# Performance work log

Measured on AMD Instinct MI355X. Metric: run time of the kernel, lower is better.

Reference implementation:

```python
import jax, jax.numpy as jnp
import numpy as np

RES = 1024
DEPTH = 2.0

def setup_inputs() -> dict:
    key = jax.random.key(0)
    k1, k2 = jax.random.split(key)
    point_cloud = jax.random.normal(k1, (32, 200000, 3), dtype=jnp.float32)
    transformation_matrices = jax.random.normal(k2, (32, 3, 4), dtype=jnp.float32)
    return {"point_cloud": point_cloud, "transformation_matrices": transformation_matrices}

def reference(point_cloud, transformation_matrices):
    B, N, _ = point_cloud.shape
    R = RES
    # homogeneous transform: (B,N,4) @ (B,4,3) -> (B,N,3)
    ones = jnp.ones((B, N, 1), dtype=point_cloud.dtype)
    pc_h = jnp.concatenate([point_cloud, ones], axis=2)
    transformed = jnp.einsum('bnk,bck->bnc', pc_h, transformation_matrices)  # (B,N,3)
    normalized = transformed / DEPTH
    # pixel coords, clamped to [0, R-1]; torch int() truncates (== floor for >=0)
    px = jnp.clip((normalized[:, :, 0] + 1.0) / 2.0 * R, 0.0, R - 1)
    py = jnp.clip((1.0 - normalized[:, :, 1]) / 2.0 * R, 0.0, R - 1)
    xi = jnp.floor(px).astype(jnp.int32)
    yi = jnp.floor(py).astype(jnp.int32)
    z = normalized[:, :, 2]
    b_ids = jnp.arange(B, dtype=jnp.int32)[:, None]
    flat_pix = (b_ids * (R * R) + yi * R + xi).reshape(-1)           # (B*N,)
    gidx = jnp.arange(B * N, dtype=jnp.int32)                        # global point index; within a batch row, larger gidx == larger j
    winners = jax.ops.segment_max(gidx, flat_pix, num_segments=B * R * R)
    valid = winners >= 0                                             # empty segments get int32 min
    safe_w = jnp.clip(winners, 0)
    depth_flat = jnp.where(valid, z.reshape(-1)[safe_w], 0.0)
    depth_map = depth_flat.reshape(B, R, R)
    # F.interpolate to the same (R,R) size with bilinear/align_corners=False is the identity map.
    return depth_map
```

## Files before the change

### kernel.cpp

```cpp
#include <hip/hip_runtime.h>

#define RES   1024
#define NPTS  200000
#define NB    32
#define PPT   8
#define BLK   512
#define NBLK  49
#define BPB   4096
#define NBAND 256
#define BANDH 4
#define BORD  4096
#define NBUCK (NB*NBAND)
#define TGRID 1024

#define OFF_AR 0
#define OFF_TM 51380224
#define OFF_BW 52985856

__global__ __launch_bounds__(256) void k_init(int4* __restrict__ bwin4)
{
    int i = blockIdx.x * 256 + threadIdx.x;
    bwin4[i] = make_int4(-1, -1, -1, -1);
}

__global__ __launch_bounds__(BLK) void k_bin(
        const float* __restrict__ pc,
        const float* __restrict__ tm,
        unsigned long long* __restrict__ arena,
        unsigned int* __restrict__ tmeta,
        int* __restrict__ bwin)
{
#pragma clang fp contract(off)
    const int b   = blockIdx.y;
    const int tid = threadIdx.x;
    const int gg  = b * NBLK + blockIdx.x;

    __shared__ int sb[BORD];
    __shared__ unsigned long long stage[BPB];
    __shared__ unsigned int hist[NBAND];
    __shared__ unsigned int lofs[NBAND];
    for (int k = tid; k < BORD; k += BLK) sb[k] = -1;
    if (tid < NBAND) hist[tid] = 0u;
    __syncthreads();

    const float* M = tm + b * 12;
    const float m0 = M[0], m1 = M[1], m2  = M[2],  m3  = M[3];
    const float m4 = M[4], m5 = M[5], m6  = M[6],  m7  = M[7];
    const float m8 = M[8], m9 = M[9], m10 = M[10], m11 = M[11];

    unsigned long long ent[PPT];
    unsigned int rb[PPT];
    const int base = blockIdx.x * BPB + tid;

    #pragma unroll
    for (int k = 0; k < PPT; ++k) {
        rb[k] = 0xFFFFFFFFu;
        int n = base + k * BLK;
        if (n < NPTS) {
            const float* p = pc + ((size_t)b * NPTS + n) * 3;
            float x = p[0], y = p[1], z = p[2];
            float tx = (x * m0 + y * m1) + (z * m2  + m3);
            float ty = (x * m4 + y * m5) + (z * m6  + m7);
            float tz = (x * m8 + y * m9) + (z * m10 + m11);
            float nx = tx * 0.5f;
            float ny = ty * 0.5f;
            float nz = tz * 0.5f;
            float px = (nx + 1.0f) * 512.0f;
            float py = (1.0f - ny) * 512.0f;
            px = fminf(fmaxf(px, 0.0f), 1023.0f);
            py = fminf(fmaxf(py, 0.0f), 1023.0f);
            int xi = (int)floorf(px);
            int yi = (int)floorf(py);

            bool border = (xi == 0) | (xi == 1023) | (yi == 0) | (yi == 1023);
            if (border) {
                int idx = (yi == 0)    ? xi
                        : (yi == 1023) ? 1024 + xi
                        : (xi == 0)    ? 2048 + yi
                                       : 3072 + yi;
                atomicMax(&sb[idx], n);
            } else {
                int bin = yi >> 2;
                unsigned r = atomicAdd(&hist[bin], 1u);
                rb[k] = ((unsigned)bin << 12) | r;
                unsigned pix = (unsigned)((yi & 3) * RES + xi);
                ent[k] = ((unsigned long long)pix << 52)
                       | ((unsigned long long)(unsigned)n << 32)
                       | (unsigned long long)__float_as_uint(nz);
            }
        }
    }
    __syncthreads();

    if (tid < 64) {
        unsigned carry = 0;
        #pragma unroll
        for (int c = 0; c < 4; ++c) {
            unsigned v = hist[c * 64 + tid];
            unsigned s = v;
            #pragma unroll
            for (int d = 1; d < 64; d <<= 1) {
                unsigned o = __shfl_up(s, d);
                if (tid >= d) s += o;
            }
            lofs[c * 64 + tid] = (s - v) + carry;
            carry += __shfl(s, 63);
        }
    }
    __syncthreads();

    if (tid < NBAND)
        tmeta[((size_t)(b * NBAND + tid)) * NBLK + blockIdx.x]
            = (lofs[tid] << 16) | hist[tid];

    #pragma unroll
    for (int k = 0; k < PPT; ++k) {
        if (rb[k] != 0xFFFFFFFFu) {
            unsigned bin = rb[k] >> 12, r = rb[k] & 4095u;
            stage[lofs[bin] + r] = ent[k];
        }
    }
    __syncthreads();

    const unsigned Ttot = lofs[NBAND - 1] + hist[NBAND - 1];
    for (unsigned k = tid; k < Ttot; k += BLK)
        arena[(size_t)gg * BPB + k] = stage[k];

    for (int k = tid; k < BORD; k += BLK) {
        int v = sb[k];
        if (v >= 0) atomicMax(&bwin[b * BORD + k], v);
    }
}

__global__ __launch_bounds__(512) void k_tile(
        const unsigned long long* __restrict__ arena,
        const unsigned int* __restrict__ tmeta,
        const int* __restrict__ bwin,
        const float* __restrict__ pc,
        const float* __restrict__ tm,
        float* __restrict__ out)
{
#pragma clang fp contract(off)
    const int tid = threadIdx.x;

    __shared__ __align__(16) unsigned long long tile[BANDH * RES];
    __shared__ unsigned int pref[NBLK + 1];
    __shared__ unsigned int sbase[NBLK];

    for (int bucket = blockIdx.x; bucket < NBUCK; bucket += TGRID) {
        const int b = bucket >> 8, band = bucket & 255;

        for (int k = tid; k < BANDH * RES; k += 512) tile[k] = 0ull;

        unsigned mv = 0;
        if (tid < NBLK)
            mv = tmeta[((size_t)(b * NBAND + band)) * NBLK + tid];
        if (tid < 64) {
            unsigned cnt = (tid < NBLK) ? (mv & 0xFFFFu) : 0u;
            unsigned s = cnt;
            #pragma unroll
            for (int d = 1; d < 64; d <<= 1) {
                unsigned o = __shfl_up(s, d);
                if (tid >= d) s += o;
            }
            if (tid < NBLK) {
                pref[tid + 1] = s;
                sbase[tid] = (unsigned)((b * NBLK + tid) * BPB) + (mv >> 16);
            }
            if (tid == 0) pref[0] = 0u;
        }
        __syncthreads();

        const unsigned T = pref[NBLK];
        for (unsigned idx = tid; idx < T; idx += 512) {
            int lo = 0, hi = NBLK - 1;
            #pragma unroll
            for (int it = 0; it < 6; ++it) {
                int mid = (lo + hi + 1) >> 1;
                if (pref[mid] <= idx) lo = mid; else hi = mid - 1;
            }
            unsigned long long e = arena[(size_t)sbase[lo] + (idx - pref[lo])];
            atomicMax(&tile[e >> 52], e & 0x000FFFFFFFFFFFFFull);
        }
        __syncthreads();

        const float* M2 = tm + b * 12 + 8;
        const float m8 = M2[0], m9 = M2[1], m10 = M2[2], m11 = M2[3];
        const int y0 = band * BANDH;
        const int* bw = bwin + b * BORD;

        for (int r = 0; r < BANDH; ++r) {
            int yi = y0 + r;
            ulonglong2 kk = ((const ulonglong2*)(tile + r * RES))[tid];
            unsigned zx = (unsigned)(kk.x & 0xFFFFFFFFull);
            unsigned zy = (unsigned)(kk.y & 0xFFFFFFFFull);

            #pragma unroll
            for (int h = 0; h < 2; ++h) {
                int xi = tid * 2 + h;
                bool isb = (yi == 0) | (yi == 1023) | (xi == 0) | (xi == 1023);
                if (isb) {
                    int n = (yi == 0)    ? bw[xi]
                          : (yi == 1023) ? bw[1024 + xi]
                          : (xi == 0)    ? bw[2048 + yi]
                                         : bw[3072 + yi];
                    float zv = 0.0f;
                    if (n >= 0) {
                        const float* p = pc + ((size_t)b * NPTS + n) * 3;
                        float t = (p[0] * m8 + p[1] * m9) + (p[2] * m10 + m11);
                        zv = t * 0.5f;
                    }
                    if (h) zy = __float_as_uint(zv); else zx = __float_as_uint(zv);
                }
            }
            unsigned long long pv = ((unsigned long long)zy << 32) | zx;
            __builtin_nontemporal_store(pv,
                (unsigned long long*)(out + ((size_t)b * RES + yi) * RES) + tid);
        }
        __syncthreads();
    }
}

extern "C" void kernel_launch(void* const* d_in, const int* in_sizes, int n_in,
                              void* d_out, int out_size, void* d_ws, size_t ws_size,
                              hipStream_t stream)
{
    const float* pc = (const float*)d_in[0];
    const float* tm = (const float*)d_in[1];
    float* out = (float*)d_out;

    char* ws = (char*)d_ws;
    unsigned long long* arena = (unsigned long long*)(ws + OFF_AR);
    unsigned int* tmeta = (unsigned int*)(ws + OFF_TM);
    int*          bwin  = (int*)         (ws + OFF_BW);

    k_init<<<(NB * BORD / 4) / 256, 256, 0, stream>>>((int4*)bwin);

    dim3 g1(NBLK, NB);
    k_bin<<<g1, BLK, 0, stream>>>(pc, tm, arena, tmeta, bwin);

    k_tile<<<TGRID, 512, 0, stream>>>(arena, tmeta, bwin, pc, tm, out);
}
```

Measured before the change: 96.87 us.

## Stage point cloud through shared memory with float4 loads; one tile block per bucket

k_bin now copies each block's points into shared memory with coalesced float4 loads instead of strided 12-byte per-thread loads. It overlays the border-winner array and the staging buffer on one 48KB buffer, and defers the border atomics until after the histogram pass. k_tile drops its grid-stride loop and launches one block per (batch, band) bucket, which adds blocks but removes the serialized iterations. The tradeoff is an extra shared-memory pass and more block launches in exchange for better global load coalescing.

```diff
diff --git a/kernel.cpp b/kernel.cpp
--- a/kernel.cpp
+++ b/kernel.cpp
@@ -10,12 +10,13 @@
 #define NBAND 256
 #define BANDH 4
 #define BORD  4096
-#define NBUCK (NB*NBAND)
-#define TGRID 1024
 
 #define OFF_AR 0
 #define OFF_TM 51380224
 #define OFF_BW 52985856
+
+#define RB_INVALID 0xFFFFFFFFu
+#define RB_BORDER  0xFFFFFFFEu
 
 __global__ __launch_bounds__(256) void k_init(int4* __restrict__ bwin4)
 {
@@ -35,11 +36,22 @@
     const int tid = threadIdx.x;
     const int gg  = b * NBLK + blockIdx.x;
 
-    __shared__ int sb[BORD];
-    __shared__ unsigned long long stage[BPB];
+    __shared__ __align__(16) char smem[49152];
     __shared__ unsigned int hist[NBAND];
     __shared__ unsigned int lofs[NBAND];
-    for (int k = tid; k < BORD; k += BLK) sb[k] = -1;
+
+    float*              pcs   = (float*)smem;
+    float4*             pcs4  = (float4*)smem;
+    int*                sb    = (int*)smem;
+    unsigned long long* stage = (unsigned long long*)(smem + 16384);
+
+    const int blk0     = blockIdx.x * BPB;
+    const int npts_blk = min(BPB, NPTS - blk0);
+    const float* pcb   = pc + (size_t)b * NPTS * 3;
+
+    const int nf4 = (npts_blk * 3) >> 2;
+    const float4* src4 = (const float4*)pcb + ((size_t)blk0 * 3 >> 2);
+    for (int i = tid; i < nf4; i += BLK) pcs4[i] = src4[i];
     if (tid < NBAND) hist[tid] = 0u;
     __syncthreads();
 
@@ -50,15 +62,13 @@
 
     unsigned long long ent[PPT];
     unsigned int rb[PPT];
-    const int base = blockIdx.x * BPB + tid;
 
     #pragma unroll
     for (int k = 0; k < PPT; ++k) {
-        rb[k] = 0xFFFFFFFFu;
-        int n = base + k * BLK;
-        if (n < NPTS) {
-            const float* p = pc + ((size_t)b * NPTS + n) * 3;
-            float x = p[0], y = p[1], z = p[2];
+        rb[k] = RB_INVALID;
+        int j = k * BLK + tid;
+        if (j < npts_blk) {
+            float x = pcs[j * 3], y = pcs[j * 3 + 1], z = pcs[j * 3 + 2];
             float tx = (x * m0 + y * m1) + (z * m2  + m3);
             float ty = (x * m4 + y * m5) + (z * m6  + m7);
             float tz = (x * m8 + y * m9) + (z * m10 + m11);
@@ -71,6 +81,7 @@
             py = fminf(fmaxf(py, 0.0f), 1023.0f);
             int xi = (int)floorf(px);
             int yi = (int)floorf(py);
+            int n  = blk0 + j;
 
             bool border = (xi == 0) | (xi == 1023) | (yi == 0) | (yi == 1023);
             if (border) {
@@ -78,7 +89,8 @@
                         : (yi == 1023) ? 1024 + xi
                         : (xi == 0)    ? 2048 + yi
                                        : 3072 + yi;
-                atomicMax(&sb[idx], n);
+                rb[k]  = RB_BORDER;
+                ent[k] = ((unsigned long long)(unsigned)idx << 32) | (unsigned)n;
             } else {
                 int bin = yi >> 2;
                 unsigned r = atomicAdd(&hist[bin], 1u);
@@ -92,6 +104,7 @@
     }
     __syncthreads();
 
+    for (int k2 = tid; k2 < BORD; k2 += BLK) sb[k2] = -1;
     if (tid < 64) {
         unsigned carry = 0;
         #pragma unroll
@@ -109,26 +122,27 @@
     }
     __syncthreads();
 
+    #pragma unroll
+    for (int k = 0; k < PPT; ++k) {
+        if (rb[k] == RB_BORDER) {
+            atomicMax(&sb[(int)(ent[k] >> 32)], (int)(unsigned)ent[k]);
+        } else if (rb[k] != RB_INVALID) {
+            unsigned bin = rb[k] >> 12, r = rb[k] & 4095u;
+            stage[lofs[bin] + r] = ent[k];
+        }
+    }
     if (tid < NBAND)
         tmeta[((size_t)(b * NBAND + tid)) * NBLK + blockIdx.x]
             = (lofs[tid] << 16) | hist[tid];
-
-    #pragma unroll
-    for (int k = 0; k < PPT; ++k) {
-        if (rb[k] != 0xFFFFFFFFu) {
-            unsigned bin = rb[k] >> 12, r = rb[k] & 4095u;
-            stage[lofs[bin] + r] = ent[k];
-        }
-    }
     __syncthreads();
 
     const unsigned Ttot = lofs[NBAND - 1] + hist[NBAND - 1];
-    for (unsigned k = tid; k < Ttot; k += BLK)
-        arena[(size_t)gg * BPB + k] = stage[k];
-
-    for (int k = tid; k < BORD; k += BLK) {
-        int v = sb[k];
-        if (v >= 0) atomicMax(&bwin[b * BORD + k], v);
+    for (unsigned k2 = tid; k2 < Ttot; k2 += BLK)
+        arena[(size_t)gg * BPB + k2] = stage[k2];
+
+    for (int k2 = tid; k2 < BORD; k2 += BLK) {
+        int v = sb[k2];
+        if (v >= 0) atomicMax(&bwin[b * BORD + k2], v);
     }
 }
 
@@ -141,83 +155,81 @@
         float* __restrict__ out)
 {
 #pragma clang fp contract(off)
+    const int bucket = blockIdx.x;
+    const int b = bucket >> 8, band = bucket & 255;
     const int tid = threadIdx.x;
 
     __shared__ __align__(16) unsigned long long tile[BANDH * RES];
     __shared__ unsigned int pref[NBLK + 1];
     __shared__ unsigned int sbase[NBLK];
 
-    for (int bucket = blockIdx.x; bucket < NBUCK; bucket += TGRID) {
-        const int b = bucket >> 8, band = bucket & 255;
-
-        for (int k = tid; k < BANDH * RES; k += 512) tile[k] = 0ull;
-
-        unsigned mv = 0;
-        if (tid < NBLK)
-            mv = tmeta[((size_t)(b * NBAND + band)) * NBLK + tid];
-        if (tid < 64) {
-            unsigned cnt = (tid < NBLK) ? (mv & 0xFFFFu) : 0u;
-            unsigned s = cnt;
-            #pragma unroll
-            for (int d = 1; d < 64; d <<= 1) {
-                unsigned o = __shfl_up(s, d);
-                if (tid >= d) s += o;
+    unsigned mv = 0;
+    if (tid < NBLK)
+        mv = tmeta[((size_t)(b * NBAND + band)) * NBLK + tid];
+
+    for (int k = tid; k < BANDH * RES; k += 512) tile[k] = 0ull;
+
+    if (tid < 64) {
+        unsigned cnt = (tid < NBLK) ? (mv & 0xFFFFu) : 0u;
+        unsigned s = cnt;
+        #pragma unroll
+        for (int d = 1; d < 64; d <<= 1) {
+            unsigned o = __shfl_up(s, d);
+            if (tid >= d) s += o;
+        }
+        if (tid < NBLK) {
+            pref[tid + 1] = s;
+            sbase[tid] = (unsigned)((b * NBLK + tid) * BPB) + (mv >> 16);
+        }
+        if (tid == 0) pref[0] = 0u;
+    }
+    __syncthreads();
+
+    const unsigned T = pref[NBLK];
+    for (unsigned idx = tid; idx < T; idx += 512) {
+        int lo = 0, hi = NBLK - 1;
+        #pragma unroll
+        for (int it = 0; it < 6; ++it) {
+            int mid = (lo + hi + 1) >> 1;
+            if (pref[mid] <= idx) lo = mid; else hi = mid - 1;
+        }
+        unsigned long long e = arena[(size_t)sbase[lo] + (idx - pref[lo])];
+        atomicMax(&tile[e >> 52], e & 0x000FFFFFFFFFFFFFull);
+    }
+    __syncthreads();
+
+    const float* M2 = tm + b * 12 + 8;
+    const float m8 = M2[0], m9 = M2[1], m10 = M2[2], m11 = M2[3];
+    const int y0 = band * BANDH;
+    const int* bw = bwin + b * BORD;
+
+    for (int r = 0; r < BANDH; ++r) {
+        int yi = y0 + r;
+        ulonglong2 kk = ((const ulonglong2*)(tile + r * RES))[tid];
+        unsigned zx = (unsigned)(kk.x & 0xFFFFFFFFull);
+        unsigned zy = (unsigned)(kk.y & 0xFFFFFFFFull);
+
+        #pragma unroll
+        for (int h = 0; h < 2; ++h) {
+            int xi = tid * 2 + h;
+            bool isb = (yi == 0) | (yi == 1023) | (xi == 0) | (xi == 1023);
+            if (isb) {
+                int n = (yi == 0)    ? bw[xi]
+                      : (yi == 1023) ? bw[1024 + xi]
+                      : (xi == 0)    ? bw[2048 + yi]
+                                     : bw[3072 + yi];
+                float zv = 0.0f;
+                if (n >= 0) {
+                    const float* p = pc + ((size_t)b * NPTS + n) * 3;
+                    float t = (p[0] * m8 + p[1] * m9) + (p[2] * m10 + m11);
+                    zv = t * 0.5f;
+                }
+                if (h) zy = __float_as_uint(zv); else zx = __float_as_uint(zv);
             }
-            if (tid < NBLK) {
-                pref[tid + 1] = s;
-                sbase[tid] = (unsigned)((b * NBLK + tid) * BPB) + (mv >> 16);
-            }
-            if (tid == 0) pref[0] = 0u;
-        }
-        __syncthreads();
-
-        const unsigned T = pref[NBLK];
-        for (unsigned idx = tid; idx < T; idx += 512) {
-            int lo = 0, hi = NBLK - 1;
-            #pragma unroll
-            for (int it = 0; it < 6; ++it) {
-                int mid = (lo + hi + 1) >> 1;
-                if (pref[mid] <= idx) lo = mid; else hi = mid - 1;
-            }
-            unsigned long long e = arena[(size_t)sbase[lo] + (idx - pref[lo])];
-            atomicMax(&tile[e >> 52], e & 0x000FFFFFFFFFFFFFull);
-        }
-        __syncthreads();
-
-        const float* M2 = tm + b * 12 + 8;
-        const float m8 = M2[0], m9 = M2[1], m10 = M2[2], m11 = M2[3];
-        const int y0 = band * BANDH;
-        const int* bw = bwin + b * BORD;
-
-        for (int r = 0; r < BANDH; ++r) {
-            int yi = y0 + r;
-            ulonglong2 kk = ((const ulonglong2*)(tile + r * RES))[tid];
-            unsigned zx = (unsigned)(kk.x & 0xFFFFFFFFull);
-            unsigned zy = (unsigned)(kk.y & 0xFFFFFFFFull);
-
-            #pragma unroll
-            for (int h = 0; h < 2; ++h) {
-                int xi = tid * 2 + h;
-                bool isb = (yi == 0) | (yi == 1023) | (xi == 0) | (xi == 1023);
-                if (isb) {
-                    int n = (yi == 0)    ? bw[xi]
-                          : (yi == 1023) ? bw[1024 + xi]
-                          : (xi == 0)    ? bw[2048 + yi]
-                                         : bw[3072 + yi];
-                    float zv = 0.0f;
-                    if (n >= 0) {
-                        const float* p = pc + ((size_t)b * NPTS + n) * 3;
-                        float t = (p[0] * m8 + p[1] * m9) + (p[2] * m10 + m11);
-                        zv = t * 0.5f;
-                    }
-                    if (h) zy = __float_as_uint(zv); else zx = __float_as_uint(zv);
-                }
-            }
-            unsigned long long pv = ((unsigned long long)zy << 32) | zx;
-            __builtin_nontemporal_store(pv,
-                (unsigned long long*)(out + ((size_t)b * RES + yi) * RES) + tid);
-        }
-        __syncthreads();
+        }
+        unsigned long long pv = ((unsigned long long)zy << 32) | zx;
+        __builtin_nontemporal_store(pv,
+            (unsigned long long*)(out + ((size_t)b * RES + yi) * RES) + tid);
     }
 }
 
@@ -239,5 +251,5 @@
     dim3 g1(NBLK, NB);
     k_bin<<<g1, BLK, 0, stream>>>(pc, tm, arena, tmeta, bwin);
 
-    k_tile<<<TGRID, 512, 0, stream>>>(arena, tmeta, bwin, pc, tm, out);
-}
+    k_tile<<<NB * NBAND, 512, 0, stream>>>(arena, tmeta, bwin, pc, tm, out);
+}
```

Result: faster. 83.46 us (median of 2 runs) (-13.8%).
